# Kernel optimization log

Measured on AMD Instinct MI355X. Metric: run time of the kernel, lower is better.

Reference implementation:

```python
import jax, jax.numpy as jnp
import numpy as np

NUM_USERS = 100000
NUM_ITEMS = 50000
EMB = 64
N_SOC = 1000000
N_RAT = 1000000
BATCH = 16384
EPS = 1e-8


def setup_inputs() -> dict:
    key = jax.random.key(0)
    ks = jax.random.split(key, 8)
    user_emb = 0.01 * jax.random.normal(ks[0], (NUM_USERS, EMB), jnp.float32)
    item_emb = 0.01 * jax.random.normal(ks[1], (NUM_ITEMS, EMB), jnp.float32)
    users = jax.random.randint(ks[2], (BATCH,), 0, NUM_USERS)
    items = jax.random.randint(ks[3], (BATCH,), 0, NUM_ITEMS)
    social_src = jax.random.randint(ks[4], (N_SOC,), 0, NUM_USERS)
    social_dst = jax.random.randint(ks[5], (N_SOC,), 0, NUM_USERS)
    like_u = jax.random.randint(ks[6], (N_RAT,), 0, NUM_USERS)
    like_i = jax.random.randint(ks[7], (N_RAT,), 0, NUM_ITEMS)
    return {"user_emb": user_emb, "item_emb": item_emb, "users": users,
            "items": items, "social_src": social_src, "social_dst": social_dst,
            "like_u": like_u, "like_i": like_i}


def _deg(idx, num):
    # node degree as float column vector [num, 1]
    return jax.ops.segment_sum(jnp.ones((idx.shape[0],), jnp.float32), idx,
                               num_segments=num)[:, None]


def _seg_mean(msg, idx, num):
    s = jax.ops.segment_sum(msg, idx, num_segments=num)
    cnt = _deg(idx, num)
    return s / jnp.maximum(cnt, 1.0)


def reference(user_emb, item_emb, users, items, social_src, social_dst, like_u, like_i):
    # degree-based self-weights (deg=0 -> 1, deg>0 -> ~0)
    user_deg = _deg(like_u, NUM_USERS)            # out-degree on 'like'
    u_sw = 1.0 - user_deg / (user_deg + EPS)
    item_deg = _deg(like_i, NUM_ITEMS)            # out-degree on 'rev_like'
    i_sw = 1.0 - item_deg / (item_deg + EPS)

    def social_conv(hu):
        # mean aggregation over user->user social edges
        return _seg_mean(hu[social_src], social_dst, NUM_USERS)

    def rating_conv(hu, hi):
        # user <- mean of liked-item embeddings, plus degree-gated self
        new_u = u_sw * hu + _seg_mean(hi[like_i], like_u, NUM_USERS)
        new_i = i_sw * hi + _seg_mean(hu[like_u], like_i, NUM_ITEMS)
        return new_u, new_i

    # layer 1
    soc1 = social_conv(user_emb)
    rat_u1, rat_i1 = rating_conv(user_emb, item_emb)
    u1 = 0.5 * soc1 + 0.5 * rat_u1
    # layer 2 (stacked on per-branch states, as in the torch code)
    soc2 = social_conv(soc1)
    rat_u2, _ = rating_conv(rat_u1, rat_i1)
    u2 = 0.5 * soc2 + 0.5 * rat_u2

    # l_user = [0, 1, 2]
    final_user = user_emb + u1 + u2
    final_item = item_emb

    latest_user = final_user[users]
    latest_item = final_item[items]
    predict = jax.nn.sigmoid(jnp.sum(latest_user * latest_item, axis=1))
    return predict, latest_user, latest_item
```

## Files before the change

kernel.cpp:

```cpp
#include <hip/hip_runtime.h>
#include <hip/hip_bf16.h>

#define NUSERS 100000
#define NITEMS 50000
#define NEDGE  1000000
#define NBATCH 16384
#define CAP_LU 320000
#define EPB    2048
#define NBLK_E ((NEDGE + EPB - 1) / EPB)
#define NBW    3125
#define GGRID  2048

#define OFF_GC     0
#define OFF_GB     768
#define OFF_GCUR   1536
#define OFF_BITS   2304
#define OFF_NEED   (OFF_BITS + 3136)
#define OFF_ZEND   (OFF_NEED + NUSERS / 4)
#define OFF_IDEG   OFF_ZEND
#define OFF_UDEG   (OFF_IDEG + NITEMS)
#define OFF_SDEG   (OFF_UDEG + NUSERS)
#define OFF_ISTART (OFF_SDEG + NUSERS)
#define OFF_USTART (OFF_ISTART + NITEMS)
#define OFF_SSTART (OFF_USTART + NUSERS)
#define OFF_PARTLI (OFF_SSTART + NUSERS)
#define OFF_PARTLU (OFF_PARTLI + NEDGE)
#define OFF_PARTSD (OFF_PARTLU + CAP_LU)
#define OFF_UEMBH  OFF_PARTLI
#define OFF_CSRLI  (OFF_UEMBH + NUSERS * 32)
#define OFF_CSRLU  (OFF_CSRLI + NEDGE)
#define OFF_RI1    (OFF_CSRLU + CAP_LU)
#define OFF_SOC1   OFF_CSRLI
#define OFF_CSRSD  (OFF_SOC1 + NUSERS * 32)
#define OFF_RU1C   (OFF_CSRSD + NEDGE)
#define OFF_RU2C   (OFF_RU1C + NBATCH * 32)
#define WS_FLOATS  (OFF_RU2C + NBATCH * 32)

typedef unsigned short u16;

__device__ __forceinline__ float bf2f(u16 h) {
    union { unsigned u; float f; } c; c.u = ((unsigned)h) << 16; return c.f;
}
__device__ __forceinline__ u16 f2bf(float f) {
    union { float f; unsigned u; } c; c.f = f;
    unsigned r = c.u + 0x7fffu + ((c.u >> 16) & 1u);
    return (u16)(r >> 16);
}
__device__ __forceinline__ void acc2(unsigned w, float& a0, float& a1) {
    a0 += bf2f((u16)(w & 0xffff));
    a1 += bf2f((u16)(w >> 16));
}

__global__ void k_slot(const int* __restrict__ users, unsigned* __restrict__ bits,
                       unsigned char* __restrict__ needed) {
    int b = blockIdx.x * blockDim.x + threadIdx.x;
    if (b < NBATCH) {
        int u = users[b];
        atomicOr(&bits[u >> 5], 1u << (u & 31));
        needed[u] = 1;
    }
}

__global__ void k_passA(const int* __restrict__ lu, const int* __restrict__ li,
                        const int* __restrict__ sd, const int* __restrict__ ss,
                        const unsigned* __restrict__ bits, int* __restrict__ gcnt,
                        unsigned char* __restrict__ needed) {
    __shared__ int lc[768];
    __shared__ unsigned sbits[NBW];
    int t = threadIdx.x;
    for (int k = t; k < 768; k += 256) lc[k] = 0;
    for (int k = t; k < NBW; k += 256) sbits[k] = bits[k];
    __syncthreads();
    int base = blockIdx.x * EPB;
    int end = base + EPB; if (end > NEDGE) end = NEDGE;
    for (int e = base + t; e < end; e += 256) {
        int item = li[e], a = lu[e], d = sd[e];
        atomicAdd(&lc[item >> 9], 1);
        if ((sbits[a >> 5] >> (a & 31)) & 1)
            atomicAdd(&lc[256 + (a >> 9)], 1);
        atomicAdd(&lc[512 + (d >> 9)], 1);
        if ((sbits[d >> 5] >> (d & 31)) & 1)
            needed[ss[e]] = 1;
    }
    __syncthreads();
    for (int k = t; k < 768; k += 256)
        if (lc[k]) atomicAdd(&gcnt[k], lc[k]);
}

__global__ void k_passB(const int* __restrict__ gcnt, int* __restrict__ gbase,
                        int* __restrict__ gcur) {
    __shared__ int s[256];
    int t = threadIdx.x;
    for (int j = 0; j < 3; ++j) {
        int v = gcnt[j * 256 + t];
        s[t] = v;
        __syncthreads();
        for (int o = 1; o < 256; o <<= 1) {
            int x = (t >= o) ? s[t - o] : 0;
            __syncthreads();
            s[t] += x;
            __syncthreads();
        }
        int ex = s[t] - v;
        gbase[j * 256 + t] = ex;
        gcur[j * 256 + t] = ex;
        __syncthreads();
    }
}

__global__ void k_passC(const int* __restrict__ lu, const int* __restrict__ li,
                        const int* __restrict__ sd, const int* __restrict__ ss,
                        const unsigned* __restrict__ bits, int* __restrict__ gcur,
                        int* __restrict__ partLI, int* __restrict__ partLU,
                        int* __restrict__ partSD) {
    __shared__ int lc[768];
    __shared__ int go[768];
    __shared__ unsigned sbits[NBW];
    int t = threadIdx.x;
    for (int k = t; k < 768; k += 256) lc[k] = 0;
    for (int k = t; k < NBW; k += 256) sbits[k] = bits[k];
    __syncthreads();
    int base = blockIdx.x * EPB;
    int end = base + EPB; if (end > NEDGE) end = NEDGE;
    unsigned mask = 0;
    int i = 0;
    for (int e = base + t; e < end; e += 256, ++i) {
        int item = li[e], a = lu[e], d = sd[e];
        atomicAdd(&lc[item >> 9], 1);
        if ((sbits[a >> 5] >> (a & 31)) & 1) {
            atomicAdd(&lc[256 + (a >> 9)], 1);
            mask |= (1u << i);
        }
        atomicAdd(&lc[512 + (d >> 9)], 1);
    }
    __syncthreads();
    for (int k = t; k < 768; k += 256) {
        go[k] = lc[k] ? atomicAdd(&gcur[k], lc[k]) : 0;
        lc[k] = 0;
    }
    __syncthreads();
    i = 0;
    for (int e = base + t; e < end; e += 256, ++i) {
        int item = li[e], a = lu[e], d = sd[e], s_ = ss[e];
        int b0 = item >> 9;
        int r0 = atomicAdd(&lc[b0], 1);
        partLI[go[b0] + r0] = (a << 9) | (item & 511);
        if (mask & (1u << i)) {
            int b1 = 256 + (a >> 9);
            int r1 = atomicAdd(&lc[b1], 1);
            partLU[go[b1] + r1] = (item << 9) | (a & 511);
        }
        int b2 = 512 + (d >> 9);
        int r2 = atomicAdd(&lc[b2], 1);
        partSD[go[b2] + r2] = (s_ << 9) | (d & 511);
    }
}

__global__ void k_passD(const int* __restrict__ gcnt, const int* __restrict__ gbase,
                        const int* __restrict__ partLI, const int* __restrict__ partLU,
                        const int* __restrict__ partSD, int* __restrict__ csrli,
                        int* __restrict__ csrlu, int* __restrict__ csrsd,
                        int* __restrict__ ideg, int* __restrict__ udeg,
                        int* __restrict__ sdeg, int* __restrict__ istart,
                        int* __restrict__ ustart, int* __restrict__ sstart) {
    __shared__ int lcnt[512], lstart[512], sb[2][512];
    int t = threadIdx.x;
    int blk = blockIdx.x, list, b;
    const int* part; int* csr; int* deg; int* start; int n;
    if (blk < 196)      { list = 0; b = blk;       part = partLI; csr = csrli; deg = ideg; start = istart; n = NITEMS; }
    else if (blk < 392) { list = 1; b = blk - 196; part = partLU; csr = csrlu; deg = udeg; start = ustart; n = NUSERS; }
    else                { list = 2; b = blk - 392; part = partSD; csr = csrsd; deg = sdeg; start = sstart; n = NUSERS; }
    int base = gbase[list * 256 + b], cnt = gcnt[list * 256 + b];
    int node0 = b << 9;
    int M = n - node0; if (M > 512) M = 512; if (M < 0) M = 0;

    lcnt[t] = 0; lcnt[t + 256] = 0;
    __syncthreads();
    for (int i = t; i < cnt; i += 256) atomicAdd(&lcnt[part[base + i] & 511], 1);
    __syncthreads();
    sb[0][t] = lcnt[t]; sb[0][t + 256] = lcnt[t + 256];
    __syncthreads();
    int pp = 0;
    for (int o = 1; o < 512; o <<= 1) {
        int np = pp ^ 1;
        for (int k = t; k < 512; k += 256) {
            int v = sb[pp][k];
            if (k >= o) v += sb[pp][k - o];
            sb[np][k] = v;
        }
        __syncthreads();
        pp = np;
    }
    for (int k = t; k < 512; k += 256) {
        int ex = sb[pp][k] - lcnt[k];
        lstart[k] = ex;
        if (k < M) { deg[node0 + k] = lcnt[k]; start[node0 + k] = base + ex; }
    }
    __syncthreads();
    lcnt[t] = 0; lcnt[t + 256] = 0;
    __syncthreads();
    for (int i = t; i < cnt; i += 256) {
        int p = part[base + i];
        int nl = p & 511;
        int r = atomicAdd(&lcnt[nl], 1);
        csr[base + lstart[nl] + r] = p >> 9;
    }
}

__global__ void k_cvt(const float* __restrict__ src, u16* __restrict__ dst) {
    int t = blockIdx.x * 256 + threadIdx.x;
    if (t >= NUSERS * 16) return;
    float4 v = ((const float4*)src)[t];
    ushort4 o;
    o.x = f2bf(v.x); o.y = f2bf(v.y); o.z = f2bf(v.z); o.w = f2bf(v.w);
    ((ushort4*)dst)[t] = o;
}

__global__ void k_gather_item(const float* __restrict__ iemb,
                              const unsigned* __restrict__ uh32,
                              const int* __restrict__ csr, const int* __restrict__ istart,
                              const int* __restrict__ ideg, unsigned* __restrict__ ri1) {
    int lane = threadIdx.x & 63;
    int wid  = blockIdx.x * 4 + (threadIdx.x >> 6);
    int nw   = gridDim.x * 4;
    int half = lane >> 5, l = lane & 31;
    for (int nA = wid * 2; nA < NITEMS; nA += nw * 2) {
        int nB = nA + 1;
        int jA = istart[nA], dA = ideg[nA];
        int jB = istart[nB], dB = ideg[nB];
        int cA = (lane < dA) ? csr[jA + lane] : 0;
        int cB = (lane < dB) ? csr[jB + lane] : 0;
        float a0=0.f,b0=0.f,a1=0.f,b1=0.f,a2=0.f,b2=0.f,a3=0.f,b3=0.f;
        float e0a=0.f,f0a=0.f,e1a=0.f,f1a=0.f,e2a=0.f,f2a=0.f,e3a=0.f,f3a=0.f;
        int kmA = dA < 64 ? dA : 64;
        int kmB = dB < 64 ? dB : 64;
        int km = kmA > kmB ? kmA : kmB;
        for (int k = 0; k < km; k += 8) {
            int q0 = k + half, q1 = k + 2 + half, q2 = k + 4 + half, q3 = k + 6 + half;
            int rA0 = __shfl(cA, q0), rA1 = __shfl(cA, q1);
            int rA2 = __shfl(cA, q2), rA3 = __shfl(cA, q3);
            int rB0 = __shfl(cB, q0), rB1 = __shfl(cB, q1);
            int rB2 = __shfl(cB, q2), rB3 = __shfl(cB, q3);
            if (q0 < kmA) acc2(uh32[rA0 * 32 + l], a0, b0);
            if (q1 < kmA) acc2(uh32[rA1 * 32 + l], a1, b1);
            if (q2 < kmA) acc2(uh32[rA2 * 32 + l], a2, b2);
            if (q3 < kmA) acc2(uh32[rA3 * 32 + l], a3, b3);
            if (q0 < kmB) acc2(uh32[rB0 * 32 + l], e0a, f0a);
            if (q1 < kmB) acc2(uh32[rB1 * 32 + l], e1a, f1a);
            if (q2 < kmB) acc2(uh32[rB2 * 32 + l], e2a, f2a);
            if (q3 < kmB) acc2(uh32[rB3 * 32 + l], e3a, f3a);
        }
        for (int j = jA + 64; j < jA + dA; j += 2) {
            int idx = j + half;
            if (idx < jA + dA) acc2(uh32[csr[idx] * 32 + l], a0, b0);
        }
        for (int j = jB + 64; j < jB + dB; j += 2) {
            int idx = j + half;
            if (idx < jB + dB) acc2(uh32[csr[idx] * 32 + l], e0a, f0a);
        }
        float sA0 = (a0 + a1) + (a2 + a3);
        float sA1 = (b0 + b1) + (b2 + b3);
        float sB0 = (e0a + e1a) + (e2a + e3a);
        float sB1 = (f0a + f1a) + (f2a + f3a);
        sA0 += __shfl_xor(sA0, 32); sA1 += __shfl_xor(sA1, 32);
        sB0 += __shfl_xor(sB0, 32); sB1 += __shfl_xor(sB1, 32);
        if (half == 0) {
            float dgf = (float)dA;
            float inv = 1.0f / fmaxf(dgf, 1.0f);
            float sw = 1.0f - dgf / (dgf + 1e-8f);
            float2 ev = ((const float2*)(iemb + nA * 64))[l];
            ri1[nA * 32 + l] = (unsigned)f2bf(sw * ev.x + sA0 * inv)
                             | ((unsigned)f2bf(sw * ev.y + sA1 * inv) << 16);
            float dgg = (float)dB;
            float inv2 = 1.0f / fmaxf(dgg, 1.0f);
            float sw2 = 1.0f - dgg / (dgg + 1e-8f);
            float2 ev2 = ((const float2*)(iemb + nB * 64))[l];
            ri1[nB * 32 + l] = (unsigned)f2bf(sw2 * ev2.x + sB0 * inv2)
                             | ((unsigned)f2bf(sw2 * ev2.y + sB1 * inv2) << 16);
        }
    }
}

__global__ void k_batch_rat(const int* __restrict__ users, const float* __restrict__ iemb,
                            const u16* __restrict__ ri1, const int* __restrict__ csr,
                            const int* __restrict__ ustart, const int* __restrict__ udeg,
                            u16* __restrict__ ru1c, u16* __restrict__ ru2c) {
    int lane = threadIdx.x & 63;
    int wid  = blockIdx.x * 4 + (threadIdx.x >> 6);
    int nw   = gridDim.x * 4;
    for (int b = wid; b < NBATCH; b += nw) {
        int u = users[b];
        int j0 = ustart[u], dg = udeg[u];
        int cv = (lane < dg) ? csr[j0 + lane] : 0;
        float p0=0.f,p1=0.f,p2=0.f,p3=0.f, q0=0.f,q1=0.f,q2=0.f,q3=0.f;
        int km = dg < 64 ? dg : 64;
        for (int k = 0; k < km; k += 4) {
            int i0 = __shfl(cv, k),     i1 = __shfl(cv, k + 1);
            int i2 = __shfl(cv, k + 2), i3 = __shfl(cv, k + 3);
            p0 += iemb[i0 * 64 + lane]; q0 += bf2f(ri1[i0 * 64 + lane]);
            if (k + 1 < km) { p1 += iemb[i1 * 64 + lane]; q1 += bf2f(ri1[i1 * 64 + lane]); }
            if (k + 2 < km) { p2 += iemb[i2 * 64 + lane]; q2 += bf2f(ri1[i2 * 64 + lane]); }
            if (k + 3 < km) { p3 += iemb[i3 * 64 + lane]; q3 += bf2f(ri1[i3 * 64 + lane]); }
        }
        for (int j = j0 + 64; j < j0 + dg; ++j) {
            int i0 = csr[j];
            p0 += iemb[i0 * 64 + lane]; q0 += bf2f(ri1[i0 * 64 + lane]);
        }
        float inv = 1.0f / fmaxf((float)dg, 1.0f);
        ru1c[b * 64 + lane] = f2bf(((p0 + p1) + (p2 + p3)) * inv);
        ru2c[b * 64 + lane] = f2bf(((q0 + q1) + (q2 + q3)) * inv);
    }
}

__global__ void k_gather_soc(const unsigned* __restrict__ uh32,
                             const int* __restrict__ csr, const int* __restrict__ sstart,
                             const int* __restrict__ sdeg,
                             const unsigned char* __restrict__ needed,
                             unsigned* __restrict__ soc1) {
    int lane = threadIdx.x & 63;
    int wid  = blockIdx.x * 4 + (threadIdx.x >> 6);
    int nw   = gridDim.x * 4;
    int half = lane >> 5, l = lane & 31;
    for (int nA = wid * 2; nA < NUSERS; nA += nw * 2) {
        int nB = nA + 1;
        unsigned short nd = *(const unsigned short*)(needed + nA);
        if (!nd) continue;
        int needA = nd & 0xff, needB = nd >> 8;
        int jA = sstart[nA], dA = needA ? sdeg[nA] : 0;
        int jB = sstart[nB], dB = needB ? sdeg[nB] : 0;
        int cA = (lane < dA) ? csr[jA + lane] : 0;
        int cB = (lane < dB) ? csr[jB + lane] : 0;
        float a0=0.f,b0=0.f,a1=0.f,b1=0.f,a2=0.f,b2=0.f,a3=0.f,b3=0.f;
        float e0a=0.f,f0a=0.f,e1a=0.f,f1a=0.f,e2a=0.f,f2a=0.f,e3a=0.f,f3a=0.f;
        int kmA = dA < 64 ? dA : 64;
        int kmB = dB < 64 ? dB : 64;
        int km = kmA > kmB ? kmA : kmB;
        for (int k = 0; k < km; k += 8) {
            int q0 = k + half, q1 = k + 2 + half, q2 = k + 4 + half, q3 = k + 6 + half;
            int rA0 = __shfl(cA, q0), rA1 = __shfl(cA, q1);
            int rA2 = __shfl(cA, q2), rA3 = __shfl(cA, q3);
            int rB0 = __shfl(cB, q0), rB1 = __shfl(cB, q1);
            int rB2 = __shfl(cB, q2), rB3 = __shfl(cB, q3);
            if (q0 < kmA) acc2(uh32[rA0 * 32 + l], a0, b0);
            if (q1 < kmA) acc2(uh32[rA1 * 32 + l], a1, b1);
            if (q2 < kmA) acc2(uh32[rA2 * 32 + l], a2, b2);
            if (q3 < kmA) acc2(uh32[rA3 * 32 + l], a3, b3);
            if (q0 < kmB) acc2(uh32[rB0 * 32 + l], e0a, f0a);
            if (q1 < kmB) acc2(uh32[rB1 * 32 + l], e1a, f1a);
            if (q2 < kmB) acc2(uh32[rB2 * 32 + l], e2a, f2a);
            if (q3 < kmB) acc2(uh32[rB3 * 32 + l], e3a, f3a);
        }
        for (int j = jA + 64; j < jA + dA; j += 2) {
            int idx = j + half;
            if (idx < jA + dA) acc2(uh32[csr[idx] * 32 + l], a0, b0);
        }
        for (int j = jB + 64; j < jB + dB; j += 2) {
            int idx = j + half;
            if (idx < jB + dB) acc2(uh32[csr[idx] * 32 + l], e0a, f0a);
        }
        float sA0 = (a0 + a1) + (a2 + a3);
        float sA1 = (b0 + b1) + (b2 + b3);
        float sB0 = (e0a + e1a) + (e2a + e3a);
        float sB1 = (f0a + f1a) + (f2a + f3a);
        sA0 += __shfl_xor(sA0, 32); sA1 += __shfl_xor(sA1, 32);
        sB0 += __shfl_xor(sB0, 32); sB1 += __shfl_xor(sB1, 32);
        if (half == 0) {
            if (needA) {
                float inv = 1.0f / fmaxf((float)dA, 1.0f);
                soc1[nA * 32 + l] = (unsigned)f2bf(sA0 * inv)
                                  | ((unsigned)f2bf(sA1 * inv) << 16);
            }
            if (needB) {
                float inv = 1.0f / fmaxf((float)dB, 1.0f);
                soc1[nB * 32 + l] = (unsigned)f2bf(sB0 * inv)
                                  | ((unsigned)f2bf(sB1 * inv) << 16);
            }
        }
    }
}

__global__ void k_final(const int* __restrict__ users, const int* __restrict__ items,
                        const float* __restrict__ uemb, const float* __restrict__ iemb,
                        const u16* __restrict__ soc1, const int* __restrict__ csr,
                        const int* __restrict__ sstart, const int* __restrict__ sdeg,
                        const u16* __restrict__ ru1c, const u16* __restrict__ ru2c,
                        const int* __restrict__ udeg, float* __restrict__ out) {
    int d   = threadIdx.x & 63;
    int wid = blockIdx.x * 4 + (threadIdx.x >> 6);
    int nw  = gridDim.x * 4;
    for (int b = wid; b < NBATCH; b += nw) {
        int u = users[b], it = items[b];
        int j0 = sstart[u], dg = sdeg[u];
        int cv = (d < dg) ? csr[j0 + d] : 0;
        float s0=0.f, s1a=0.f, s2a=0.f, s3a=0.f;
        int km = dg < 64 ? dg : 64;
        for (int k = 0; k < km; k += 4) {
            int c0 = __shfl(cv, k),     c1 = __shfl(cv, k + 1);
            int c2 = __shfl(cv, k + 2), c3 = __shfl(cv, k + 3);
            s0 += bf2f(soc1[c0 * 64 + d]);
            if (k + 1 < km) s1a += bf2f(soc1[c1 * 64 + d]);
            if (k + 2 < km) s2a += bf2f(soc1[c2 * 64 + d]);
            if (k + 3 < km) s3a += bf2f(soc1[c3 * 64 + d]);
        }
        for (int j = j0 + 64; j < j0 + dg; ++j)
            s0 += bf2f(soc1[csr[j] * 64 + d]);
        float s2 = ((s0 + s1a) + (s2a + s3a)) / fmaxf((float)dg, 1.0f);
        float ud = (float)udeg[u];
        float usw = 1.0f - ud / (ud + 1e-8f);
        float ue = uemb[u * 64 + d];
        float s1 = bf2f(soc1[u * 64 + d]);
        float r1 = usw * ue + bf2f(ru1c[b * 64 + d]);
        float r2 = usw * r1 + bf2f(ru2c[b * 64 + d]);
        float fu = ue + 0.5f * (s1 + r1) + 0.5f * (s2 + r2);
        float iv = iemb[it * 64 + d];
        out[NBATCH + b * 64 + d]               = fu;
        out[NBATCH + NBATCH * 64 + b * 64 + d] = iv;
        float p = fu * iv;
        #pragma unroll
        for (int o = 32; o > 0; o >>= 1) p += __shfl_down(p, o);
        if (d == 0) out[b] = 1.0f / (1.0f + __expf(-p));
    }
}

extern "C" void kernel_launch(void* const* d_in, const int* in_sizes, int n_in,
                              void* d_out, int out_size, void* d_ws, size_t ws_size,
                              hipStream_t stream) {
    const float* uemb  = (const float*)d_in[0];
    const float* iemb  = (const float*)d_in[1];
    const int*   users = (const int*)d_in[2];
    const int*   items = (const int*)d_in[3];
    const int*   ssrc  = (const int*)d_in[4];
    const int*   sdst  = (const int*)d_in[5];
    const int*   lu    = (const int*)d_in[6];
    const int*   li    = (const int*)d_in[7];
    float* out = (float*)d_out;

    if (ws_size < (size_t)WS_FLOATS * 4) return;

    int*           W      = (int*)d_ws;
    int*           gcnt   = W + OFF_GC;
    int*           gbase  = W + OFF_GB;
    int*           gcur   = W + OFF_GCUR;
    unsigned*      bits   = (unsigned*)(W + OFF_BITS);
    unsigned char* needed = (unsigned char*)(W + OFF_NEED);
    int*           ideg   = W + OFF_IDEG;
    int*           udeg   = W + OFF_UDEG;
    int*           sdeg   = W + OFF_SDEG;
    int*           istart = W + OFF_ISTART;
    int*           ustart = W + OFF_USTART;
    int*           sstart = W + OFF_SSTART;
    int*           partLI = W + OFF_PARTLI;
    int*           partLU = W + OFF_PARTLU;
    int*           partSD = W + OFF_PARTSD;
    u16*           uembh  = (u16*)(W + OFF_UEMBH);
    int*           csrli  = W + OFF_CSRLI;
    int*           csrlu  = W + OFF_CSRLU;
    int*           csrsd  = W + OFF_CSRSD;
    u16*           ri1    = (u16*)(W + OFF_RI1);
    u16*           soc1   = (u16*)(W + OFF_SOC1);
    u16*           ru1c   = (u16*)(W + OFF_RU1C);
    u16*           ru2c   = (u16*)(W + OFF_RU2C);

    hipMemsetAsync(d_ws, 0, (size_t)OFF_ZEND * 4, stream);

    const int B = 256;

    k_slot<<<(NBATCH + B - 1) / B, B, 0, stream>>>(users, bits, needed);
    k_passA<<<NBLK_E, B, 0, stream>>>(lu, li, sdst, ssrc, bits, gcnt, needed);
    k_passB<<<1, B, 0, stream>>>(gcnt, gbase, gcur);
    k_passC<<<NBLK_E, B, 0, stream>>>(lu, li, sdst, ssrc, bits, gcur,
                                      partLI, partLU, partSD);
    k_passD<<<588, B, 0, stream>>>(gcnt, gbase, partLI, partLU, partSD,
                                   csrli, csrlu, csrsd, ideg, udeg, sdeg,
                                   istart, ustart, sstart);

    k_cvt<<<(NUSERS * 16 + B - 1) / B, B, 0, stream>>>(uemb, uembh);

    k_gather_item<<<GGRID, B, 0, stream>>>(iemb, (const unsigned*)uembh,
                                           csrli, istart, ideg, (unsigned*)ri1);
    k_batch_rat<<<GGRID, B, 0, stream>>>(users, iemb, ri1, csrlu, ustart,
                                         udeg, ru1c, ru2c);
    k_gather_soc<<<GGRID, B, 0, stream>>>((const unsigned*)uembh, csrsd,
                                          sstart, sdeg, needed, (unsigned*)soc1);

    k_final<<<GGRID, B, 0, stream>>>(users, items, uemb, iemb, soc1,
                                     csrsd, sstart, sdeg, ru1c, ru2c, udeg, out);
}
```

Before: 296.8 us.

## Use 16-byte row gathers and unconditional clamped loads in CSR aggregation kernels

The item and social gather kernels now assign 8 lanes per neighbor row, each loading a uint4 (8 bf16 values), so a wavefront processes 8 neighbors per load instruction instead of 2. Partial sums are combined with xor-shuffle reductions across the lane groups. The batch kernels issue 8 loads per iteration with indices clamped to a valid slot and masking only at the accumulate step, so loads are no longer predicated and more memory requests can be in flight. The cost is extra shuffle-reduction work, more registers per thread, and redundant loads of the clamped row.

Result: faster. 274.0 us (-7.7%).

```diff
diff --git a/kernel.cpp b/kernel.cpp
--- a/kernel.cpp
+++ b/kernel.cpp
@@ -50,6 +50,10 @@
     a0 += bf2f((u16)(w & 0xffff));
     a1 += bf2f((u16)(w >> 16));
 }
+__device__ __forceinline__ void acc8(uint4 w, float* a) {
+    acc2(w.x, a[0], a[1]); acc2(w.y, a[2], a[3]);
+    acc2(w.z, a[4], a[5]); acc2(w.w, a[6], a[7]);
+}
 
 __global__ void k_slot(const int* __restrict__ users, unsigned* __restrict__ bits,
                        unsigned char* __restrict__ needed) {
@@ -216,6 +220,34 @@
     ((ushort4*)dst)[t] = o;
 }
 
+__device__ __forceinline__ void item_store(int n, int dg, const float* __restrict__ iemb,
+                                           unsigned* __restrict__ ri1, int l8,
+                                           float s0, float s1, float s2, float s3,
+                                           float s4, float s5, float s6, float s7) {
+    float dgf = (float)dg;
+    float inv = 1.0f / fmaxf(dgf, 1.0f);
+    float sw  = 1.0f - dgf / (dgf + 1e-8f);
+    float4 e0 = ((const float4*)(iemb + n * 64))[l8 * 2];
+    float4 e1 = ((const float4*)(iemb + n * 64))[l8 * 2 + 1];
+    uint4 o;
+    o.x = (unsigned)f2bf(sw * e0.x + s0 * inv) | ((unsigned)f2bf(sw * e0.y + s1 * inv) << 16);
+    o.y = (unsigned)f2bf(sw * e0.z + s2 * inv) | ((unsigned)f2bf(sw * e0.w + s3 * inv) << 16);
+    o.z = (unsigned)f2bf(sw * e1.x + s4 * inv) | ((unsigned)f2bf(sw * e1.y + s5 * inv) << 16);
+    o.w = (unsigned)f2bf(sw * e1.z + s6 * inv) | ((unsigned)f2bf(sw * e1.w + s7 * inv) << 16);
+    ((uint4*)(ri1 + n * 32))[l8] = o;
+}
+__device__ __forceinline__ void soc_store(int n, int dg, unsigned* __restrict__ soc1, int l8,
+                                          float s0, float s1, float s2, float s3,
+                                          float s4, float s5, float s6, float s7) {
+    float inv = 1.0f / fmaxf((float)dg, 1.0f);
+    uint4 o;
+    o.x = (unsigned)f2bf(s0 * inv) | ((unsigned)f2bf(s1 * inv) << 16);
+    o.y = (unsigned)f2bf(s2 * inv) | ((unsigned)f2bf(s3 * inv) << 16);
+    o.z = (unsigned)f2bf(s4 * inv) | ((unsigned)f2bf(s5 * inv) << 16);
+    o.w = (unsigned)f2bf(s6 * inv) | ((unsigned)f2bf(s7 * inv) << 16);
+    ((uint4*)(soc1 + n * 32))[l8] = o;
+}
+
 __global__ void k_gather_item(const float* __restrict__ iemb,
                               const unsigned* __restrict__ uh32,
                               const int* __restrict__ csr, const int* __restrict__ istart,
@@ -223,61 +255,61 @@
     int lane = threadIdx.x & 63;
     int wid  = blockIdx.x * 4 + (threadIdx.x >> 6);
     int nw   = gridDim.x * 4;
-    int half = lane >> 5, l = lane & 31;
+    int g = lane >> 3, l8 = lane & 7;
     for (int nA = wid * 2; nA < NITEMS; nA += nw * 2) {
         int nB = nA + 1;
         int jA = istart[nA], dA = ideg[nA];
         int jB = istart[nB], dB = ideg[nB];
         int cA = (lane < dA) ? csr[jA + lane] : 0;
         int cB = (lane < dB) ? csr[jB + lane] : 0;
-        float a0=0.f,b0=0.f,a1=0.f,b1=0.f,a2=0.f,b2=0.f,a3=0.f,b3=0.f;
-        float e0a=0.f,f0a=0.f,e1a=0.f,f1a=0.f,e2a=0.f,f2a=0.f,e3a=0.f,f3a=0.f;
         int kmA = dA < 64 ? dA : 64;
         int kmB = dB < 64 ? dB : 64;
-        int km = kmA > kmB ? kmA : kmB;
-        for (int k = 0; k < km; k += 8) {
-            int q0 = k + half, q1 = k + 2 + half, q2 = k + 4 + half, q3 = k + 6 + half;
-            int rA0 = __shfl(cA, q0), rA1 = __shfl(cA, q1);
-            int rA2 = __shfl(cA, q2), rA3 = __shfl(cA, q3);
-            int rB0 = __shfl(cB, q0), rB1 = __shfl(cB, q1);
-            int rB2 = __shfl(cB, q2), rB3 = __shfl(cB, q3);
-            if (q0 < kmA) acc2(uh32[rA0 * 32 + l], a0, b0);
-            if (q1 < kmA) acc2(uh32[rA1 * 32 + l], a1, b1);
-            if (q2 < kmA) acc2(uh32[rA2 * 32 + l], a2, b2);
-            if (q3 < kmA) acc2(uh32[rA3 * 32 + l], a3, b3);
-            if (q0 < kmB) acc2(uh32[rB0 * 32 + l], e0a, f0a);
-            if (q1 < kmB) acc2(uh32[rB1 * 32 + l], e1a, f1a);
-            if (q2 < kmB) acc2(uh32[rB2 * 32 + l], e2a, f2a);
-            if (q3 < kmB) acc2(uh32[rB3 * 32 + l], e3a, f3a);
-        }
-        for (int j = jA + 64; j < jA + dA; j += 2) {
-            int idx = j + half;
-            if (idx < jA + dA) acc2(uh32[csr[idx] * 32 + l], a0, b0);
-        }
-        for (int j = jB + 64; j < jB + dB; j += 2) {
-            int idx = j + half;
-            if (idx < jB + dB) acc2(uh32[csr[idx] * 32 + l], e0a, f0a);
-        }
-        float sA0 = (a0 + a1) + (a2 + a3);
-        float sA1 = (b0 + b1) + (b2 + b3);
-        float sB0 = (e0a + e1a) + (e2a + e3a);
-        float sB1 = (f0a + f1a) + (f2a + f3a);
-        sA0 += __shfl_xor(sA0, 32); sA1 += __shfl_xor(sA1, 32);
-        sB0 += __shfl_xor(sB0, 32); sB1 += __shfl_xor(sB1, 32);
-        if (half == 0) {
-            float dgf = (float)dA;
-            float inv = 1.0f / fmaxf(dgf, 1.0f);
-            float sw = 1.0f - dgf / (dgf + 1e-8f);
-            float2 ev = ((const float2*)(iemb + nA * 64))[l];
-            ri1[nA * 32 + l] = (unsigned)f2bf(sw * ev.x + sA0 * inv)
-                             | ((unsigned)f2bf(sw * ev.y + sA1 * inv) << 16);
-            float dgg = (float)dB;
-            float inv2 = 1.0f / fmaxf(dgg, 1.0f);
-            float sw2 = 1.0f - dgg / (dgg + 1e-8f);
-            float2 ev2 = ((const float2*)(iemb + nB * 64))[l];
-            ri1[nB * 32 + l] = (unsigned)f2bf(sw2 * ev2.x + sB0 * inv2)
-                             | ((unsigned)f2bf(sw2 * ev2.y + sB1 * inv2) << 16);
-        }
+        int clA = kmA > 0 ? kmA - 1 : 0;
+        int clB = kmB > 0 ? kmB - 1 : 0;
+        int km  = kmA > kmB ? kmA : kmB;
+        float aA[8] = {0.f,0.f,0.f,0.f,0.f,0.f,0.f,0.f};
+        float aB[8] = {0.f,0.f,0.f,0.f,0.f,0.f,0.f,0.f};
+        for (int k = 0; k < km; k += 16) {
+            int q0 = k + g, q1 = k + 8 + g;
+            int iA0 = q0 < kmA ? q0 : clA;
+            int iA1 = q1 < kmA ? q1 : clA;
+            int iB0 = q0 < kmB ? q0 : clB;
+            int iB1 = q1 < kmB ? q1 : clB;
+            int rA0 = __shfl(cA, iA0), rA1 = __shfl(cA, iA1);
+            int rB0 = __shfl(cB, iB0), rB1 = __shfl(cB, iB1);
+            uint4 wA0 = *(const uint4*)(uh32 + rA0 * 32 + l8 * 4);
+            uint4 wA1 = *(const uint4*)(uh32 + rA1 * 32 + l8 * 4);
+            uint4 wB0 = *(const uint4*)(uh32 + rB0 * 32 + l8 * 4);
+            uint4 wB1 = *(const uint4*)(uh32 + rB1 * 32 + l8 * 4);
+            if (q0 < kmA) acc8(wA0, aA);
+            if (q1 < kmA) acc8(wA1, aA);
+            if (q0 < kmB) acc8(wB0, aB);
+            if (q1 < kmB) acc8(wB1, aB);
+        }
+        for (int k = 64; k < dA; k += 8) {
+            int q = k + g; int idx = q < dA ? q : dA - 1;
+            int r = csr[jA + idx];
+            uint4 w = *(const uint4*)(uh32 + r * 32 + l8 * 4);
+            if (q < dA) acc8(w, aA);
+        }
+        for (int k = 64; k < dB; k += 8) {
+            int q = k + g; int idx = q < dB ? q : dB - 1;
+            int r = csr[jB + idx];
+            uint4 w = *(const uint4*)(uh32 + r * 32 + l8 * 4);
+            if (q < dB) acc8(w, aB);
+        }
+        #pragma unroll
+        for (int off = 8; off <= 32; off <<= 1) {
+            #pragma unroll
+            for (int m = 0; m < 8; ++m) {
+                aA[m] += __shfl_xor(aA[m], off);
+                aB[m] += __shfl_xor(aB[m], off);
+            }
+        }
+        if (g == 0)
+            item_store(nA, dA, iemb, ri1, l8, aA[0],aA[1],aA[2],aA[3],aA[4],aA[5],aA[6],aA[7]);
+        else if (g == 1)
+            item_store(nB, dB, iemb, ri1, l8, aB[0],aB[1],aB[2],aB[3],aB[4],aB[5],aB[6],aB[7]);
     }
 }
 
@@ -292,15 +324,34 @@
         int u = users[b];
         int j0 = ustart[u], dg = udeg[u];
         int cv = (lane < dg) ? csr[j0 + lane] : 0;
+        int km = dg < 64 ? dg : 64;
+        int cl = km > 0 ? km - 1 : 0;
         float p0=0.f,p1=0.f,p2=0.f,p3=0.f, q0=0.f,q1=0.f,q2=0.f,q3=0.f;
-        int km = dg < 64 ? dg : 64;
-        for (int k = 0; k < km; k += 4) {
-            int i0 = __shfl(cv, k),     i1 = __shfl(cv, k + 1);
-            int i2 = __shfl(cv, k + 2), i3 = __shfl(cv, k + 3);
-            p0 += iemb[i0 * 64 + lane]; q0 += bf2f(ri1[i0 * 64 + lane]);
-            if (k + 1 < km) { p1 += iemb[i1 * 64 + lane]; q1 += bf2f(ri1[i1 * 64 + lane]); }
-            if (k + 2 < km) { p2 += iemb[i2 * 64 + lane]; q2 += bf2f(ri1[i2 * 64 + lane]); }
-            if (k + 3 < km) { p3 += iemb[i3 * 64 + lane]; q3 += bf2f(ri1[i3 * 64 + lane]); }
+        for (int k = 0; k < km; k += 8) {
+            int x1 = k+1 < km ? k+1 : cl, x2 = k+2 < km ? k+2 : cl;
+            int x3 = k+3 < km ? k+3 : cl, x4 = k+4 < km ? k+4 : cl;
+            int x5 = k+5 < km ? k+5 : cl, x6 = k+6 < km ? k+6 : cl;
+            int x7 = k+7 < km ? k+7 : cl;
+            int i0 = __shfl(cv, k),  i1 = __shfl(cv, x1);
+            int i2 = __shfl(cv, x2), i3 = __shfl(cv, x3);
+            int i4 = __shfl(cv, x4), i5 = __shfl(cv, x5);
+            int i6 = __shfl(cv, x6), i7 = __shfl(cv, x7);
+            float t0 = iemb[i0 * 64 + lane], t1 = iemb[i1 * 64 + lane];
+            float t2 = iemb[i2 * 64 + lane], t3 = iemb[i3 * 64 + lane];
+            float t4 = iemb[i4 * 64 + lane], t5 = iemb[i5 * 64 + lane];
+            float t6 = iemb[i6 * 64 + lane], t7 = iemb[i7 * 64 + lane];
+            float r0 = bf2f(ri1[i0 * 64 + lane]), r1 = bf2f(ri1[i1 * 64 + lane]);
+            float r2 = bf2f(ri1[i2 * 64 + lane]), r3 = bf2f(ri1[i3 * 64 + lane]);
+            float r4 = bf2f(ri1[i4 * 64 + lane]), r5 = bf2f(ri1[i5 * 64 + lane]);
+            float r6 = bf2f(ri1[i6 * 64 + lane]), r7 = bf2f(ri1[i7 * 64 + lane]);
+            p0 += t0; q0 += r0;
+            if (k+1 < km) { p1 += t1; q1 += r1; }
+            if (k+2 < km) { p2 += t2; q2 += r2; }
+            if (k+3 < km) { p3 += t3; q3 += r3; }
+            if (k+4 < km) { p0 += t4; q0 += r4; }
+            if (k+5 < km) { p1 += t5; q1 += r5; }
+            if (k+6 < km) { p2 += t6; q2 += r6; }
+            if (k+7 < km) { p3 += t7; q3 += r7; }
         }
         for (int j = j0 + 64; j < j0 + dg; ++j) {
             int i0 = csr[j];
@@ -320,7 +371,7 @@
     int lane = threadIdx.x & 63;
     int wid  = blockIdx.x * 4 + (threadIdx.x >> 6);
     int nw   = gridDim.x * 4;
-    int half = lane >> 5, l = lane & 31;
+    int g = lane >> 3, l8 = lane & 7;
     for (int nA = wid * 2; nA < NUSERS; nA += nw * 2) {
         int nB = nA + 1;
         unsigned short nd = *(const unsigned short*)(needed + nA);
@@ -330,52 +381,54 @@
         int jB = sstart[nB], dB = needB ? sdeg[nB] : 0;
         int cA = (lane < dA) ? csr[jA + lane] : 0;
         int cB = (lane < dB) ? csr[jB + lane] : 0;
-        float a0=0.f,b0=0.f,a1=0.f,b1=0.f,a2=0.f,b2=0.f,a3=0.f,b3=0.f;
-        float e0a=0.f,f0a=0.f,e1a=0.f,f1a=0.f,e2a=0.f,f2a=0.f,e3a=0.f,f3a=0.f;
         int kmA = dA < 64 ? dA : 64;
         int kmB = dB < 64 ? dB : 64;
-        int km = kmA > kmB ? kmA : kmB;
-        for (int k = 0; k < km; k += 8) {
-            int q0 = k + half, q1 = k + 2 + half, q2 = k + 4 + half, q3 = k + 6 + half;
-            int rA0 = __shfl(cA, q0), rA1 = __shfl(cA, q1);
-            int rA2 = __shfl(cA, q2), rA3 = __shfl(cA, q3);
-            int rB0 = __shfl(cB, q0), rB1 = __shfl(cB, q1);
-            int rB2 = __shfl(cB, q2), rB3 = __shfl(cB, q3);
-            if (q0 < kmA) acc2(uh32[rA0 * 32 + l], a0, b0);
-            if (q1 < kmA) acc2(uh32[rA1 * 32 + l], a1, b1);
-            if (q2 < kmA) acc2(uh32[rA2 * 32 + l], a2, b2);
-            if (q3 < kmA) acc2(uh32[rA3 * 32 + l], a3, b3);
-            if (q0 < kmB) acc2(uh32[rB0 * 32 + l], e0a, f0a);
-            if (q1 < kmB) acc2(uh32[rB1 * 32 + l], e1a, f1a);
-            if (q2 < kmB) acc2(uh32[rB2 * 32 + l], e2a, f2a);
-            if (q3 < kmB) acc2(uh32[rB3 * 32 + l], e3a, f3a);
-        }
-        for (int j = jA + 64; j < jA + dA; j += 2) {
-            int idx = j + half;
-            if (idx < jA + dA) acc2(uh32[csr[idx] * 32 + l], a0, b0);
-        }
-        for (int j = jB + 64; j < jB + dB; j += 2) {
-            int idx = j + half;
-            if (idx < jB + dB) acc2(uh32[csr[idx] * 32 + l], e0a, f0a);
-        }
-        float sA0 = (a0 + a1) + (a2 + a3);
-        float sA1 = (b0 + b1) + (b2 + b3);
-        float sB0 = (e0a + e1a) + (e2a + e3a);
-        float sB1 = (f0a + f1a) + (f2a + f3a);
-        sA0 += __shfl_xor(sA0, 32); sA1 += __shfl_xor(sA1, 32);
-        sB0 += __shfl_xor(sB0, 32); sB1 += __shfl_xor(sB1, 32);
-        if (half == 0) {
-            if (needA) {
-                float inv = 1.0f / fmaxf((float)dA, 1.0f);
-                soc1[nA * 32 + l] = (unsigned)f2bf(sA0 * inv)
-                                  | ((unsigned)f2bf(sA1 * inv) << 16);
+        int clA = kmA > 0 ? kmA - 1 : 0;
+        int clB = kmB > 0 ? kmB - 1 : 0;
+        int km  = kmA > kmB ? kmA : kmB;
+        float aA[8] = {0.f,0.f,0.f,0.f,0.f,0.f,0.f,0.f};
+        float aB[8] = {0.f,0.f,0.f,0.f,0.f,0.f,0.f,0.f};
+        for (int k = 0; k < km; k += 16) {
+            int q0 = k + g, q1 = k + 8 + g;
+            int iA0 = q0 < kmA ? q0 : clA;
+            int iA1 = q1 < kmA ? q1 : clA;
+            int iB0 = q0 < kmB ? q0 : clB;
+            int iB1 = q1 < kmB ? q1 : clB;
+            int rA0 = __shfl(cA, iA0), rA1 = __shfl(cA, iA1);
+            int rB0 = __shfl(cB, iB0), rB1 = __shfl(cB, iB1);
+            uint4 wA0 = *(const uint4*)(uh32 + rA0 * 32 + l8 * 4);
+            uint4 wA1 = *(const uint4*)(uh32 + rA1 * 32 + l8 * 4);
+            uint4 wB0 = *(const uint4*)(uh32 + rB0 * 32 + l8 * 4);
+            uint4 wB1 = *(const uint4*)(uh32 + rB1 * 32 + l8 * 4);
+            if (q0 < kmA) acc8(wA0, aA);
+            if (q1 < kmA) acc8(wA1, aA);
+            if (q0 < kmB) acc8(wB0, aB);
+            if (q1 < kmB) acc8(wB1, aB);
+        }
+        for (int k = 64; k < dA; k += 8) {
+            int q = k + g; int idx = q < dA ? q : dA - 1;
+            int r = csr[jA + idx];
+            uint4 w = *(const uint4*)(uh32 + r * 32 + l8 * 4);
+            if (q < dA) acc8(w, aA);
+        }
+        for (int k = 64; k < dB; k += 8) {
+            int q = k + g; int idx = q < dB ? q : dB - 1;
+            int r = csr[jB + idx];
+            uint4 w = *(const uint4*)(uh32 + r * 32 + l8 * 4);
+            if (q < dB) acc8(w, aB);
+        }
+        #pragma unroll
+        for (int off = 8; off <= 32; off <<= 1) {
+            #pragma unroll
+            for (int m = 0; m < 8; ++m) {
+                aA[m] += __shfl_xor(aA[m], off);
+                aB[m] += __shfl_xor(aB[m], off);
             }
-            if (needB) {
-                float inv = 1.0f / fmaxf((float)dB, 1.0f);
-                soc1[nB * 32 + l] = (unsigned)f2bf(sB0 * inv)
-                                  | ((unsigned)f2bf(sB1 * inv) << 16);
-            }
-        }
+        }
+        if (g == 0 && needA)
+            soc_store(nA, dA, soc1, l8, aA[0],aA[1],aA[2],aA[3],aA[4],aA[5],aA[6],aA[7]);
+        else if (g == 1 && needB)
+            soc_store(nB, dB, soc1, l8, aB[0],aB[1],aB[2],aB[3],aB[4],aB[5],aB[6],aB[7]);
     }
 }
 
@@ -392,15 +445,30 @@
         int u = users[b], it = items[b];
         int j0 = sstart[u], dg = sdeg[u];
         int cv = (d < dg) ? csr[j0 + d] : 0;
+        int km = dg < 64 ? dg : 64;
+        int cl = km > 0 ? km - 1 : 0;
         float s0=0.f, s1a=0.f, s2a=0.f, s3a=0.f;
-        int km = dg < 64 ? dg : 64;
-        for (int k = 0; k < km; k += 4) {
-            int c0 = __shfl(cv, k),     c1 = __shfl(cv, k + 1);
-            int c2 = __shfl(cv, k + 2), c3 = __shfl(cv, k + 3);
-            s0 += bf2f(soc1[c0 * 64 + d]);
-            if (k + 1 < km) s1a += bf2f(soc1[c1 * 64 + d]);
-            if (k + 2 < km) s2a += bf2f(soc1[c2 * 64 + d]);
-            if (k + 3 < km) s3a += bf2f(soc1[c3 * 64 + d]);
+        for (int k = 0; k < km; k += 8) {
+            int x1 = k+1 < km ? k+1 : cl, x2 = k+2 < km ? k+2 : cl;
+            int x3 = k+3 < km ? k+3 : cl, x4 = k+4 < km ? k+4 : cl;
+            int x5 = k+5 < km ? k+5 : cl, x6 = k+6 < km ? k+6 : cl;
+            int x7 = k+7 < km ? k+7 : cl;
+            int c0 = __shfl(cv, k),  c1 = __shfl(cv, x1);
+            int c2 = __shfl(cv, x2), c3 = __shfl(cv, x3);
+            int c4 = __shfl(cv, x4), c5 = __shfl(cv, x5);
+            int c6 = __shfl(cv, x6), c7 = __shfl(cv, x7);
+            float f0 = bf2f(soc1[c0 * 64 + d]), f1 = bf2f(soc1[c1 * 64 + d]);
+            float f2 = bf2f(soc1[c2 * 64 + d]), f3 = bf2f(soc1[c3 * 64 + d]);
+            float f4 = bf2f(soc1[c4 * 64 + d]), f5 = bf2f(soc1[c5 * 64 + d]);
+            float f6 = bf2f(soc1[c6 * 64 + d]), f7 = bf2f(soc1[c7 * 64 + d]);
+            s0 += f0;
+            if (k+1 < km) s1a += f1;
+            if (k+2 < km) s2a += f2;
+            if (k+3 < km) s3a += f3;
+            if (k+4 < km) s0  += f4;
+            if (k+5 < km) s1a += f5;
+            if (k+6 < km) s2a += f6;
+            if (k+7 < km) s3a += f7;
         }
         for (int j = j0 + 64; j < j0 + dg; ++j)
             s0 += bf2f(soc1[csr[j] * 64 + d]);
```
